# Kernel optimization log

Measured on AMD Instinct MI355X. Metric: run time of the kernel, lower is better.

Reference implementation:

```python
import jax, jax.numpy as jnp
import numpy as np

B, N, S, T_STEPS = 8, 150, 22, 1000
E = 2 * N - 1  # 299
M = 32


def quat_mul(a, b):
    # Hamilton product, quats as (w, x, y, z)
    aw, ax, ay, az = a[..., 0], a[..., 1], a[..., 2], a[..., 3]
    bw, bx, by, bz = b[..., 0], b[..., 1], b[..., 2], b[..., 3]
    return jnp.stack([
        aw * bw - ax * bx - ay * by - az * bz,
        aw * bx + ax * bw + ay * bz - az * by,
        aw * by - ax * bz + ay * bw + az * bx,
        aw * bz + ax * by - ay * bx + az * bw,
    ], axis=-1)


def quat_conj(q):
    return q * jnp.array([1.0, -1.0, -1.0, -1.0], q.dtype)


def quat_rotate(q, v):
    # rotate vector v by unit quaternion q
    w, qv = q[..., :1], q[..., 1:]
    t = 2.0 * jnp.cross(qv, v)
    return v + w * t + jnp.cross(qv, t)


def egnn_layer(q, x, h, e, mask_f, Wm, bm, Wf, bf, Wq, bq):
    Bb, Nn = h.shape[0], h.shape[-2]
    eye = jnp.eye(Nn, dtype=h.dtype)
    mm = mask_f[:, :, None] * mask_f[:, None, :] * (1.0 - eye)  # [B,N,N]
    n_nodes = mask_f.sum(-1)  # [B]
    q_i = q[:, :, None, :]
    q_j = q[:, None, :, :]
    x_i = x[:, :, None, :]
    x_j = x[:, None, :, :]
    qj_inv = quat_conj(q_j)
    diff = x_i - x_j                              # [B,N,N,3]
    local_x = quat_rotate(qj_inv, diff)           # R_j^T (x_i - x_j)
    local_q = quat_mul(quat_mul(qj_inv, q_i), q_j)  # q_j^-1 q_i q_j
    d2 = jnp.sum(diff * diff, -1)                 # [B,N,N]
    dot = jnp.abs(jnp.sum(q_i * q_j, -1))         # [B,N,N]
    hi = jnp.broadcast_to(h[:, :, None, :], (Bb, Nn, Nn, h.shape[-1]))
    hj = jnp.broadcast_to(h[:, None, :, :], (Bb, Nn, Nn, h.shape[-1]))
    feat = jnp.concatenate([hi, hj, e, local_x, local_q, d2[..., None], dot[..., None]], -1)
    m = (feat @ Wm + bm) * mm[..., None]          # [B,N,N,M]
    o = jnp.concatenate([h, m.sum(-2)], -1) @ Wf + bf
    delta = (m @ Wq + bq) * mm[..., None]         # [B,N,N,6]
    upd_x = (quat_rotate(q_j, local_x + delta[..., 3:]) + x_j).sum(-2) \
        / (n_nodes[:, None, None] - 1.0)
    vec_q = jnp.concatenate([jnp.zeros_like(delta[..., :1]), delta[..., :3]], -1)
    s = (local_q + quat_mul(local_q, vec_q)).sum(-2)  # [B,N,4]
    local_upd_q = s / jnp.maximum(jnp.linalg.norm(s, axis=-1, keepdims=True), 1e-12)
    upd_q = quat_mul(quat_mul(q, local_upd_q), quat_conj(q))
    return upd_q, upd_x, o


def relposenc():
    r = jnp.arange(N)
    rel = N - 1 + (r[:, None] - r[None, :])
    return jax.nn.one_hot(rel, E, dtype=jnp.float32)  # [N,N,E]


def setup_inputs() -> dict:
    key = jax.random.key(0)
    ks = jax.random.split(key, 32)
    quats = jax.random.normal(ks[0], (B, N, 4), dtype=jnp.float32)
    quats = quats / jnp.linalg.norm(quats, axis=-1, keepdims=True)
    trans = jax.random.normal(ks[1], (B, N, 3), dtype=jnp.float32) * 10.0
    features = jax.random.uniform(ks[2], (B, N, S), dtype=jnp.float32)
    mask = jnp.ones((B, N), dtype=bool)
    inp = {"quats": quats, "trans": trans, "features": features, "mask": mask, "t": 250}
    # (message_in, feature_in, feature_out) per layer; H1=30, I=64
    dims = [(2 * 30 + E + 9, 30 + M, 64), (2 * 64 + E + 9, 64 + M, 64),
            (2 * 64 + E + 9, 64 + M, 64), (2 * 64 + E + 9, 64 + M, 1)]
    k = 3
    for i, (mi, fi, fo) in enumerate(dims, 1):
        inp[f"wm{i}"] = jax.random.normal(ks[k], (mi, M), dtype=jnp.float32) / np.float32(np.sqrt(mi)); k += 1
        inp[f"bm{i}"] = jnp.zeros((M,), jnp.float32)
        inp[f"wf{i}"] = jax.random.normal(ks[k], (fi, fo), dtype=jnp.float32) / np.float32(np.sqrt(fi)); k += 1
        inp[f"bf{i}"] = jnp.zeros((fo,), jnp.float32)
        inp[f"wq{i}"] = jax.random.normal(ks[k], (M, 6), dtype=jnp.float32) / np.float32(np.sqrt(M)); k += 1
        inp[f"bq{i}"] = jnp.zeros((6,), jnp.float32)
    return inp


def reference(quats, trans, features,
              wm1, bm1, wf1, bf1, wq1, bq1,
              wm2, bm2, wf2, bf2, wq2, bq2,
              wm3, bm3, wf3, bf3, wq3, bq3,
              wm4, bm4, wf4, bf4, wq4, bq4,
              mask, t):
    mask_f = mask.astype(quats.dtype)
    ft = jnp.full((B, N, 1), t / T_STEPS, dtype=quats.dtype)
    h = jnp.concatenate([quats, trans, features, ft], -1)  # [B,N,30]
    e = jnp.broadcast_to(relposenc()[None], (B, N, N, E))
    q, x = quats, trans
    q, x, i1 = egnn_layer(q, x, h, e, mask_f, wm1, bm1, wf1, bf1, wq1, bq1)
    q, x, i2 = egnn_layer(q, x, jax.nn.relu(i1), e, mask_f, wm2, bm2, wf2, bf2, wq2, bq2)
    q, x, i3 = egnn_layer(q, x, jax.nn.relu(i2), e, mask_f, wm3, bm3, wf3, bf3, wq3, bq3)
    q, x, _ = egnn_layer(q, x, jax.nn.relu(i3), e, mask_f, wm4, bm4, wf4, bf4, wq4, bq4)
    return jnp.concatenate([q, x], -1)  # tensor_7 of final frames [B,N,7]
```

## Files before the change

kernel.cpp:

```cpp
#include <hip/hip_runtime.h>
#include <math.h>

#define NB 8
#define NN 150
#define NE 299
#define NNODE (NB*NN)

struct Quat { float w, x, y, z; };

__device__ inline Quat qmul(Quat a, Quat b) {
    Quat r;
    r.w = a.w*b.w - a.x*b.x - a.y*b.y - a.z*b.z;
    r.x = a.w*b.x + a.x*b.w + a.y*b.z - a.z*b.y;
    r.y = a.w*b.y - a.x*b.z + a.y*b.w + a.z*b.x;
    r.z = a.w*b.z + a.x*b.y - a.y*b.x + a.z*b.w;
    return r;
}
__device__ inline Quat qconj(Quat a) { return Quat{a.w, -a.x, -a.y, -a.z}; }

__device__ inline float3 qrot(Quat q, float3 v) {
    float tx = 2.f*(q.y*v.z - q.z*v.y);
    float ty = 2.f*(q.z*v.x - q.x*v.z);
    float tz = 2.f*(q.x*v.y - q.y*v.x);
    float cx = q.y*tz - q.z*ty;
    float cy = q.z*tx - q.x*tz;
    float cz = q.x*ty - q.y*tx;
    float3 r;
    r.x = v.x + q.w*tx + cx;
    r.y = v.y + q.w*ty + cy;
    r.z = v.z + q.w*tz + cz;
    return r;
}

struct InitArgs {
    const float* quats; const float* trans; const float* feats; const int* tptr;
    const float* wm[4]; const float* wq[4];
    const float* bm1; const float* bq1;
    float* h; float* A; float* C0; float* Ad; float* Cd0;
    float* P; float* Ed; float* Gq;
};

__global__ __launch_bounds__(256) void init_kernel(InitArgs a)
{
    __shared__ float sh[8][30];
    __shared__ float sA[8][32];
    __shared__ float sC[8][32];
    __shared__ float sPS[256];
    const int tid = threadIdx.x;
    const int blk = blockIdx.x;

    if (blk < 150) {
        const int nodeBase = blk*8;
        for (int idx = tid; idx < 8*30; idx += 256) {
            const int nl = idx / 30;
            const int d  = idx - nl*30;
            const int n  = nodeBase + nl;
            float v;
            if      (d < 4)  v = a.quats[n*4 + d];
            else if (d < 7)  v = a.trans[n*3 + (d-4)];
            else if (d < 29) v = a.feats[n*22 + (d-7)];
            else             v = (float)a.tptr[0] * (1.0f/1000.0f);
            sh[nl][d] = v;
            a.h[n*64 + d] = v;
        }
        __syncthreads();
        {
            const int nl = tid >> 5;
            const int k  = tid & 31;
            const int n  = nodeBase + nl;
            float av = a.bm1[k], cv = 0.f;
#pragma unroll
            for (int d = 0; d < 30; ++d) {
                const float hv = sh[nl][d];
                av = fmaf(hv, a.wm[0][d*32 + k], av);
                cv = fmaf(hv, a.wm[0][(30+d)*32 + k], cv);
            }
            a.A[n*32 + k]  = av;
            a.C0[n*32 + k] = cv;
            sA[nl][k] = av;
            sC[nl][k] = cv;
        }
        __syncthreads();
        if (tid < 96) {
            const int half = (tid >= 48) ? 1 : 0;
            const int idx  = tid - half*48;
            const int nl = idx / 6;
            const int d  = idx - nl*6;
            const float* src = half ? sC[nl] : sA[nl];
            float acc = half ? 0.f : a.bq1[d];
#pragma unroll
            for (int k = 0; k < 32; ++k) acc = fmaf(src[k], a.wq[0][k*6 + d], acc);
            (half ? a.Cd0 : a.Ad)[(nodeBase+nl)*8 + d] = acc;
        }
    } else if (blk < 154) {
        const int l = blk - 150;
        const int HDl = (l == 0) ? 30 : 64;
        const float* E = a.wm[l] + 2*HDl*32;
        float* Pl = a.P + l*9600;
        const int g = tid >> 5, k = tid & 31;
        const int r0 = g*38;
        float part = 0.f;
        for (int r = r0; r < r0+38 && r < NE; ++r) part += E[r*32 + k];
        sPS[g*32 + k] = part;
        __syncthreads();
        float run = 0.f;
        for (int gg = 0; gg < g; ++gg) run += sPS[gg*32 + k];
        const int rw = (r0+38 < 300) ? r0+38 : 300;
        for (int r = r0; r < rw; ++r) {
            Pl[r*32 + k] = run;
            if (r < NE) run += E[r*32 + k];
        }
    } else if (blk < 158) {
        const int l = blk - 154;
        const int HDl = (l == 0) ? 30 : 64;
        const float* E  = a.wm[l] + 2*HDl*32;
        const float* Wq = a.wq[l];
        if (tid < 54) {
            const int t = tid/6, d = tid - t*6;
            float acc = 0.f;
#pragma unroll
            for (int k = 0; k < 32; ++k) acc = fmaf(E[(NE+t)*32 + k], Wq[k*6 + d], acc);
            a.Gq[l*64 + t*6 + d] = acc;
        }
    } else {
        const int bb = blk - 158;
        const int l = bb / 25;
        const int rbase = (bb % 25) * 12;
        const int HDl = (l == 0) ? 30 : 64;
        const float* E  = a.wm[l] + 2*HDl*32;
        const float* Wq = a.wq[l];
        if (tid < 72) {
            const int rr = tid/6, d = tid - rr*6;
            const int r = rbase + rr;
            if (r < NE) {
                float acc = 0.f;
#pragma unroll
                for (int k = 0; k < 32; ++k) acc = fmaf(E[r*32 + k], Wq[k*6 + d], acc);
                a.Ed[l*2400 + r*8 + d] = acc;
            }
        }
    }
}

struct PairArgs {
    const float* qcur; const float* xcur;
    const float* hbuf; const float* Abuf;
    const float* Cin;  const float* Adin; const float* Cdin;
    const float* Ed;   const float* Gq;   const float* P;
    const float* wm;   const float* wf;   const float* bf;
    const float* wmN;  const float* bmN;
    const float* wqN;  const float* bqN;
    float* hout; float* Aout; float* Adout;
    float* Cout; float* Cdout;
    float* qout; float* xout; float* dout;
};

template<int HD, bool COMPUTE_O, bool WRITE_OUT>
__global__ __launch_bounds__(192, 4) void pair_kernel(PairArgs a)
{
    constexpr int STR  = 196;
    constexpr int NROW = COMPUTE_O ? 32 : 7;
    constexpr int NV   = COMPUTE_O ? 16 : 7;
    __shared__ __align__(16) float sMat[NROW*STR];
    __shared__ float sWmG[COMPUTE_O ? 288 : 4];
    __shared__ float sPr[192];
    __shared__ float sTot[16];
    __shared__ float sCs[32];
    __shared__ float sHi[64], sO[64], sMs[32];
    __shared__ float sGq[54], sAd[6];
    __shared__ float sA2[32], sC2[32];

    const int tid   = threadIdx.x;
    const int nodeI = blockIdx.x;
    const int b     = nodeI / NN;
    const int i     = nodeI - b*NN;

    if (COMPUTE_O) {
        for (int idx = tid; idx < 288; idx += 192) sWmG[idx] = a.wm[(2*HD+NE)*32 + idx];
        for (int idx = tid; idx < HD;  idx += 192) sHi[idx]  = a.hbuf[nodeI*64 + idx];
    }
    if (tid < 54) sGq[tid] = a.Gq[tid];
    if (tid >= 64 && tid < 70) sAd[tid-64] = a.Adin[nodeI*8 + (tid-64)];
    __syncthreads();

    const Quat  qi = {a.qcur[nodeI*4+0], a.qcur[nodeI*4+1],
                      a.qcur[nodeI*4+2], a.qcur[nodeI*4+3]};
    const float3 xi = {a.xcur[nodeI*3+0], a.xcur[nodeI*3+1], a.xcur[nodeI*3+2]};

    float vals[NV];
#pragma unroll
    for (int v = 0; v < NV; ++v) vals[v] = 0.f;

    const int j = tid;
    Quat qj = {1.f,0.f,0.f,0.f};
    const float mm = (j == i) ? 0.f : 1.f;
    if (j < NN) {
        const int nodeJ = b*NN + j;
        qj = Quat{a.qcur[nodeJ*4+0], a.qcur[nodeJ*4+1],
                  a.qcur[nodeJ*4+2], a.qcur[nodeJ*4+3]};
        float3 xj = {a.xcur[nodeJ*3+0], a.xcur[nodeJ*3+1], a.xcur[nodeJ*3+2]};
        float3 diff = {xi.x - xj.x, xi.y - xj.y, xi.z - xj.z};
        Quat qjc = qconj(qj);
        float3 lx = qrot(qjc, diff);
        Quat lq = qmul(qmul(qjc, qi), qj);
        const float d2 = diff.x*diff.x + diff.y*diff.y + diff.z*diff.z;
        const float dt = fabsf(qi.w*qj.w + qi.x*qj.x + qi.y*qj.y + qi.z*qj.z);
        const float g[9] = {lx.x, lx.y, lx.z, lq.w, lq.x, lq.y, lq.z, d2, dt};

        const float4* cd4 = (const float4*)(a.Cdin + nodeJ*8);
        const float4* ed4 = (const float4*)(a.Ed + (NN-1 + i - j)*8);
        const float4 c0 = cd4[0], c1 = cd4[1];
        const float4 e0 = ed4[0], e1 = ed4[1];
        float delta[6];
        delta[0] = sAd[0] + c0.x + e0.x;
        delta[1] = sAd[1] + c0.y + e0.y;
        delta[2] = sAd[2] + c0.z + e0.z;
        delta[3] = sAd[3] + c0.w + e0.w;
        delta[4] = sAd[4] + c1.x + e1.x;
        delta[5] = sAd[5] + c1.y + e1.y;
#pragma unroll
        for (int t = 0; t < 9; ++t) {
            const float gv = g[t];
#pragma unroll
            for (int d = 0; d < 6; ++d)
                delta[d] = fmaf(gv, sGq[t*6 + d], delta[d]);
        }
#pragma unroll
        for (int d = 0; d < 6; ++d) delta[d] *= mm;

        constexpr int vo = COMPUTE_O ? 9 : 0;
        if (COMPUTE_O) {
#pragma unroll
            for (int t = 0; t < 9; ++t) vals[t] = g[t]*mm;
        }
        float3 dv = {delta[3], delta[4], delta[5]};
        float3 rd = qrot(qj, dv);
        vals[vo+0] = rd.x; vals[vo+1] = rd.y; vals[vo+2] = rd.z;
        Quat vq = {0.f, delta[0], delta[1], delta[2]};
        Quat sp = qmul(lq, vq);
        vals[vo+3] = lq.w + sp.w;
        vals[vo+4] = lq.x + sp.x;
        vals[vo+5] = lq.y + sp.y;
        vals[vo+6] = lq.z + sp.z;
    }

#pragma unroll
    for (int v = 0; v < NV; ++v) sMat[v*STR + tid] = vals[v];
    if (COMPUTE_O) {
        if (j < NN) {
            const float4* c4p = (const float4*)(a.Cin + (b*NN+j)*32);
#pragma unroll
            for (int q = 0; q < 4; ++q) {
                const float4 c = c4p[q];
                sMat[(16+4*q+0)*STR + tid] = c.x*mm;
                sMat[(16+4*q+1)*STR + tid] = c.y*mm;
                sMat[(16+4*q+2)*STR + tid] = c.z*mm;
                sMat[(16+4*q+3)*STR + tid] = c.w*mm;
            }
        } else {
#pragma unroll
            for (int r = 16; r < 32; ++r) sMat[r*STR + tid] = 0.f;
        }
    }
    __syncthreads();
    if (tid < 4*NROW) {
        const int ch = tid >> 2, q4 = tid & 3;
        const float4* row = (const float4*)(sMat + ch*STR + q4*48);
        float s0 = 0.f, s1 = 0.f, s2 = 0.f, s3 = 0.f;
#pragma unroll
        for (int it = 0; it < 12; ++it) {
            const float4 r = row[it];
            s0 += r.x; s1 += r.y; s2 += r.z; s3 += r.w;
        }
        sPr[tid] = (s0+s1) + (s2+s3);
    }
    __syncthreads();

    if (COMPUTE_O) {
        if (j < NN) {
            const float4* c4p = (const float4*)(a.Cin + (b*NN+j)*32);
#pragma unroll
            for (int q = 0; q < 4; ++q) {
                const float4 c = c4p[4+q];
                sMat[(4*q+0)*STR + tid] = c.x*mm;
                sMat[(4*q+1)*STR + tid] = c.y*mm;
                sMat[(4*q+2)*STR + tid] = c.z*mm;
                sMat[(4*q+3)*STR + tid] = c.w*mm;
            }
        } else {
#pragma unroll
            for (int r = 0; r < 16; ++r) sMat[r*STR + tid] = 0.f;
        }
        __syncthreads();
        if (tid < 64) {
            const int ch = tid >> 2, q4 = tid & 3;
            const float4* row = (const float4*)(sMat + ch*STR + q4*48);
            float s0 = 0.f, s1 = 0.f, s2 = 0.f, s3 = 0.f;
#pragma unroll
            for (int it = 0; it < 12; ++it) {
                const float4 r = row[it];
                s0 += r.x; s1 += r.y; s2 += r.z; s3 += r.w;
            }
            sPr[128 + tid] = (s0+s1) + (s2+s3);
        }
        __syncthreads();
    }

    if (COMPUTE_O) {
        if (tid < 16)
            sTot[tid] = (sPr[4*tid] + sPr[4*tid+1]) + (sPr[4*tid+2] + sPr[4*tid+3]);
        else if (tid < 32) {
            const int c = tid - 16, o4 = 64 + 4*c;
            sCs[c] = (sPr[o4] + sPr[o4+1]) + (sPr[o4+2] + sPr[o4+3]);
        } else if (tid < 48) {
            const int c = tid - 16, o4 = 128 + 4*(tid-32);
            sCs[c] = (sPr[o4] + sPr[o4+1]) + (sPr[o4+2] + sPr[o4+3]);
        }
    } else {
        if (tid < 7)
            sTot[tid] = (sPr[4*tid] + sPr[4*tid+1]) + (sPr[4*tid+2] + sPr[4*tid+3]);
    }
    __syncthreads();

    if (COMPUTE_O) {
        if (tid < 32) {
            const int k = tid;
            float ms = 149.f*a.Abuf[nodeI*32 + k] + sCs[k]
                     + a.P[(i+NN)*32 + k] - a.P[i*32 + k]
                     - a.wm[(2*HD + (NN-1))*32 + k];
#pragma unroll
            for (int t = 0; t < 9; ++t) ms = fmaf(sTot[t], sWmG[t*32 + k], ms);
            sMs[k] = ms;
        }
        __syncthreads();
        if (tid < 64) {
            float acc0 = a.bf[tid], acc1 = 0.f;
#pragma unroll 8
            for (int d = 0; d < HD; d += 2) {
                acc0 = fmaf(sHi[d],   a.wf[d*64 + tid],     acc0);
                acc1 = fmaf(sHi[d+1], a.wf[(d+1)*64 + tid], acc1);
            }
#pragma unroll 8
            for (int k = 0; k < 32; k += 2) {
                acc0 = fmaf(sMs[k],   a.wf[(HD+k)*64 + tid],   acc0);
                acc1 = fmaf(sMs[k+1], a.wf[(HD+k+1)*64 + tid], acc1);
            }
            sO[tid] = acc0 + acc1;
        }
    }

    if (tid == 0) {
        constexpr int XO = COMPUTE_O ? 9 : 0;
        const float inv = 1.0f / (float)(NN - 1);
        const float ux0 = ((float)NN * xi.x + sTot[XO+0]) * inv;
        const float ux1 = ((float)NN * xi.y + sTot[XO+1]) * inv;
        const float ux2 = ((float)NN * xi.z + sTot[XO+2]) * inv;
        Quat s = {sTot[XO+3], sTot[XO+4], sTot[XO+5], sTot[XO+6]};
        const float nrm = sqrtf(s.w*s.w + s.x*s.x + s.y*s.y + s.z*s.z);
        const float invn = 1.0f / fmaxf(nrm, 1e-12f);
        Quat u = {s.w*invn, s.x*invn, s.y*invn, s.z*invn};
        Quat uq = qmul(qmul(qi, u), qconj(qi));
        if (WRITE_OUT) {
            float* op = a.dout + nodeI*7;
            op[0] = uq.w; op[1] = uq.x; op[2] = uq.y; op[3] = uq.z;
            op[4] = ux0;  op[5] = ux1;  op[6] = ux2;
        } else {
            a.qout[nodeI*4+0] = uq.w; a.qout[nodeI*4+1] = uq.x;
            a.qout[nodeI*4+2] = uq.y; a.qout[nodeI*4+3] = uq.z;
            a.xout[nodeI*3+0] = ux0;  a.xout[nodeI*3+1] = ux1;
            a.xout[nodeI*3+2] = ux2;
        }
    }

    if (COMPUTE_O) {
        __syncthreads();
        if (tid < 64) {
            const float hn = fmaxf(sO[tid], 0.f);
            sHi[tid] = hn;
            a.hout[nodeI*64 + tid] = hn;
        }
        __syncthreads();
        if (tid < 64) {
            const int k   = tid & 31;
            const int off = (tid >= 32) ? 64 : 0;
            float acc = (tid < 32) ? a.bmN[k] : 0.f;
#pragma unroll
            for (int d = 0; d < 64; ++d) acc = fmaf(sHi[d], a.wmN[(off+d)*32 + k], acc);
            if (tid < 32) { a.Aout[nodeI*32 + k] = acc; sA2[k] = acc; }
            else          { a.Cout[nodeI*32 + k] = acc; sC2[k] = acc; }
        }
        __syncthreads();
        if (tid < 12) {
            const int half = (tid >= 6) ? 1 : 0;
            const int d = tid - half*6;
            const float* src = half ? sC2 : sA2;
            float acc = half ? 0.f : a.bqN[d];
#pragma unroll
            for (int k = 0; k < 32; ++k) acc = fmaf(src[k], a.wqN[k*6 + d], acc);
            (half ? a.Cdout : a.Adout)[nodeI*8 + d] = acc;
        }
    }
}


extern "C" void kernel_launch(void* const* d_in, const int* in_sizes, int n_in,
                              void* d_out, int out_size, void* d_ws, size_t ws_size,
                              hipStream_t stream) {
    const float* wm[4] = {(const float*)d_in[5],  (const float*)d_in[11],
                          (const float*)d_in[17], (const float*)d_in[23]};
    const float* bm[4] = {(const float*)d_in[6],  (const float*)d_in[12],
                          (const float*)d_in[18], (const float*)d_in[24]};
    const float* wf[4] = {(const float*)d_in[7],  (const float*)d_in[13],
                          (const float*)d_in[19], (const float*)d_in[25]};
    const float* bf[4] = {(const float*)d_in[8],  (const float*)d_in[14],
                          (const float*)d_in[20], (const float*)d_in[26]};
    const float* wq[4] = {(const float*)d_in[9],  (const float*)d_in[15],
                          (const float*)d_in[21], (const float*)d_in[27]};
    const float* bq[4] = {(const float*)d_in[10], (const float*)d_in[16],
                          (const float*)d_in[22], (const float*)d_in[28]};

    float* ws = (float*)d_ws;
    float* h   = ws;
    float* A   = h   + NNODE*64;
    float* C0  = A   + NNODE*32;
    float* C1  = C0  + NNODE*32;
    float* Ad  = C1  + NNODE*32;
    float* Cd0 = Ad  + NNODE*8;
    float* Cd1 = Cd0 + NNODE*8;
    float* qA  = Cd1 + NNODE*8;
    float* xA  = qA  + NNODE*4;
    float* qB  = xA  + NNODE*3;
    float* xB  = qB  + NNODE*4;
    float* Pp  = xB  + NNODE*3;
    float* Edp = Pp  + 4*9600;
    float* Gqp = Edp + 4*2400;

    InitArgs ia;
    ia.quats = (const float*)d_in[0];
    ia.trans = (const float*)d_in[1];
    ia.feats = (const float*)d_in[2];
    ia.tptr  = (const int*)d_in[4];
    for (int l = 0; l < 4; ++l) { ia.wm[l] = wm[l]; ia.wq[l] = wq[l]; }
    ia.bm1 = bm[0]; ia.bq1 = bq[0];
    ia.h = h; ia.A = A; ia.C0 = C0; ia.Ad = Ad; ia.Cd0 = Cd0;
    ia.P = Pp; ia.Ed = Edp; ia.Gq = Gqp;
    init_kernel<<<dim3(258), dim3(256), 0, stream>>>(ia);

    PairArgs p;
    p.hout = h; p.Aout = A; p.Adout = Ad;
    p.dout = (float*)d_out;

    p.qcur = (const float*)d_in[0]; p.xcur = (const float*)d_in[1];
    p.hbuf = h; p.Abuf = A; p.Cin = C0; p.Adin = Ad; p.Cdin = Cd0;
    p.Ed = Edp + 0*2400; p.Gq = Gqp + 0*64; p.P = Pp + 0*9600;
    p.wm = wm[0]; p.wf = wf[0]; p.bf = bf[0];
    p.wmN = wm[1]; p.bmN = bm[1]; p.wqN = wq[1]; p.bqN = bq[1];
    p.Cout = C1; p.Cdout = Cd1;
    p.qout = qA; p.xout = xA;
    pair_kernel<30, true, false><<<dim3(NNODE), dim3(192), 0, stream>>>(p);

    p.qcur = qA; p.xcur = xA;
    p.Cin = C1; p.Cdin = Cd1;
    p.Ed = Edp + 1*2400; p.Gq = Gqp + 1*64; p.P = Pp + 1*9600;
    p.wm = wm[1]; p.wf = wf[1]; p.bf = bf[1];
    p.wmN = wm[2]; p.bmN = bm[2]; p.wqN = wq[2]; p.bqN = bq[2];
    p.Cout = C0; p.Cdout = Cd0;
    p.qout = qB; p.xout = xB;
    pair_kernel<64, true, false><<<dim3(NNODE), dim3(192), 0, stream>>>(p);

    p.qcur = qB; p.xcur = xB;
    p.Cin = C0; p.Cdin = Cd0;
    p.Ed = Edp + 2*2400; p.Gq = Gqp + 2*64; p.P = Pp + 2*9600;
    p.wm = wm[2]; p.wf = wf[2]; p.bf = bf[2];
    p.wmN = wm[3]; p.bmN = bm[3]; p.wqN = wq[3]; p.bqN = bq[3];
    p.Cout = C1; p.Cdout = Cd1;
    p.qout = qA; p.xout = xA;
    pair_kernel<64, true, false><<<dim3(NNODE), dim3(192), 0, stream>>>(p);

    p.qcur = qA; p.xcur = xA;
    p.Cin = C1; p.Cdin = Cd1;
    p.Ed = Edp + 3*2400; p.Gq = Gqp + 3*64; p.P = Pp + 3*9600;
    p.wm = wm[3]; p.wf = wf[3]; p.bf = bf[3];
    p.wmN = wm[3]; p.bmN = bm[3]; p.wqN = wq[3]; p.bqN = bq[3];
    p.Cout = C0; p.Cdout = Cd0;
    p.qout = nullptr; p.xout = nullptr;
    pair_kernel<64, false, true><<<dim3(NNODE), dim3(192), 0, stream>>>(p);
}
```

Before: 167.5 us.

## Fold init kernel into first pair kernel and precompute next-layer tables in-line

```diff
diff --git a/kernel.cpp b/kernel.cpp
--- a/kernel.cpp
+++ b/kernel.cpp
@@ -32,130 +32,22 @@
     return r;
 }
 
-struct InitArgs {
-    const float* quats; const float* trans; const float* feats; const int* tptr;
-    const float* wm[4]; const float* wq[4];
-    const float* bm1; const float* bq1;
-    float* h; float* A; float* C0; float* Ad; float* Cd0;
-    float* P; float* Ed; float* Gq;
-};
-
-__global__ __launch_bounds__(256) void init_kernel(InitArgs a)
-{
-    __shared__ float sh[8][30];
-    __shared__ float sA[8][32];
-    __shared__ float sC[8][32];
-    __shared__ float sPS[256];
-    const int tid = threadIdx.x;
-    const int blk = blockIdx.x;
-
-    if (blk < 150) {
-        const int nodeBase = blk*8;
-        for (int idx = tid; idx < 8*30; idx += 256) {
-            const int nl = idx / 30;
-            const int d  = idx - nl*30;
-            const int n  = nodeBase + nl;
-            float v;
-            if      (d < 4)  v = a.quats[n*4 + d];
-            else if (d < 7)  v = a.trans[n*3 + (d-4)];
-            else if (d < 29) v = a.feats[n*22 + (d-7)];
-            else             v = (float)a.tptr[0] * (1.0f/1000.0f);
-            sh[nl][d] = v;
-            a.h[n*64 + d] = v;
-        }
-        __syncthreads();
-        {
-            const int nl = tid >> 5;
-            const int k  = tid & 31;
-            const int n  = nodeBase + nl;
-            float av = a.bm1[k], cv = 0.f;
-#pragma unroll
-            for (int d = 0; d < 30; ++d) {
-                const float hv = sh[nl][d];
-                av = fmaf(hv, a.wm[0][d*32 + k], av);
-                cv = fmaf(hv, a.wm[0][(30+d)*32 + k], cv);
-            }
-            a.A[n*32 + k]  = av;
-            a.C0[n*32 + k] = cv;
-            sA[nl][k] = av;
-            sC[nl][k] = cv;
-        }
-        __syncthreads();
-        if (tid < 96) {
-            const int half = (tid >= 48) ? 1 : 0;
-            const int idx  = tid - half*48;
-            const int nl = idx / 6;
-            const int d  = idx - nl*6;
-            const float* src = half ? sC[nl] : sA[nl];
-            float acc = half ? 0.f : a.bq1[d];
-#pragma unroll
-            for (int k = 0; k < 32; ++k) acc = fmaf(src[k], a.wq[0][k*6 + d], acc);
-            (half ? a.Cd0 : a.Ad)[(nodeBase+nl)*8 + d] = acc;
-        }
-    } else if (blk < 154) {
-        const int l = blk - 150;
-        const int HDl = (l == 0) ? 30 : 64;
-        const float* E = a.wm[l] + 2*HDl*32;
-        float* Pl = a.P + l*9600;
-        const int g = tid >> 5, k = tid & 31;
-        const int r0 = g*38;
-        float part = 0.f;
-        for (int r = r0; r < r0+38 && r < NE; ++r) part += E[r*32 + k];
-        sPS[g*32 + k] = part;
-        __syncthreads();
-        float run = 0.f;
-        for (int gg = 0; gg < g; ++gg) run += sPS[gg*32 + k];
-        const int rw = (r0+38 < 300) ? r0+38 : 300;
-        for (int r = r0; r < rw; ++r) {
-            Pl[r*32 + k] = run;
-            if (r < NE) run += E[r*32 + k];
-        }
-    } else if (blk < 158) {
-        const int l = blk - 154;
-        const int HDl = (l == 0) ? 30 : 64;
-        const float* E  = a.wm[l] + 2*HDl*32;
-        const float* Wq = a.wq[l];
-        if (tid < 54) {
-            const int t = tid/6, d = tid - t*6;
-            float acc = 0.f;
-#pragma unroll
-            for (int k = 0; k < 32; ++k) acc = fmaf(E[(NE+t)*32 + k], Wq[k*6 + d], acc);
-            a.Gq[l*64 + t*6 + d] = acc;
-        }
-    } else {
-        const int bb = blk - 158;
-        const int l = bb / 25;
-        const int rbase = (bb % 25) * 12;
-        const int HDl = (l == 0) ? 30 : 64;
-        const float* E  = a.wm[l] + 2*HDl*32;
-        const float* Wq = a.wq[l];
-        if (tid < 72) {
-            const int rr = tid/6, d = tid - rr*6;
-            const int r = rbase + rr;
-            if (r < NE) {
-                float acc = 0.f;
-#pragma unroll
-                for (int k = 0; k < 32; ++k) acc = fmaf(E[r*32 + k], Wq[k*6 + d], acc);
-                a.Ed[l*2400 + r*8 + d] = acc;
-            }
-        }
-    }
-}
-
 struct PairArgs {
     const float* qcur; const float* xcur;
+    const float* feats; const int* tptr;
     const float* hbuf; const float* Abuf;
     const float* Cin;  const float* Adin; const float* Cdin;
     const float* Ed;   const float* Gq;   const float* P;
-    const float* wm;   const float* wf;   const float* bf;
-    const float* wmN;  const float* bmN;
-    const float* wqN;  const float* bqN;
+    const float* wm;   const float* bmT;  const float* wqT; const float* bqT;
+    const float* wf;   const float* bf;
+    const float* wmN;  const float* bmN;  const float* wqN; const float* bqN;
     float* hout; float* Aout; float* Adout;
     float* Cout; float* Cdout;
+    float* PN; float* EdN; float* GqN;
     float* qout; float* xout; float* dout;
 };
 
-template<int HD, bool COMPUTE_O, bool WRITE_OUT>
+template<int HD, bool COMPUTE_O, bool WRITE_OUT, bool FIRST>
 __global__ __launch_bounds__(192, 4) void pair_kernel(PairArgs a)
 {
     constexpr int STR  = 196;
@@ -169,64 +61,162 @@
     __shared__ float sHi[64], sO[64], sMs[32];
     __shared__ float sGq[54], sAd[6];
     __shared__ float sA2[32], sC2[32];
+    __shared__ float sWq[FIRST ? 192 : 1];
+    __shared__ float sWmC[FIRST ? 960 : 1];
+    __shared__ float sEtot[FIRST ? 32 : 1];
 
     const int tid   = threadIdx.x;
     const int nodeI = blockIdx.x;
     const int b     = nodeI / NN;
     const int i     = nodeI - b*NN;
+    const int j     = tid;
+    const float* Etab = a.wm + 2*HD*32;
 
     if (COMPUTE_O) {
         for (int idx = tid; idx < 288; idx += 192) sWmG[idx] = a.wm[(2*HD+NE)*32 + idx];
-        for (int idx = tid; idx < HD;  idx += 192) sHi[idx]  = a.hbuf[nodeI*64 + idx];
-    }
-    if (tid < 54) sGq[tid] = a.Gq[tid];
-    if (tid >= 64 && tid < 70) sAd[tid-64] = a.Adin[nodeI*8 + (tid-64)];
+        if (!FIRST)
+            for (int idx = tid; idx < HD; idx += 192) sHi[idx] = a.hbuf[nodeI*64 + idx];
+    }
+    if (FIRST) {
+        sWq[tid] = a.wqT[tid];
+        for (int idx = tid; idx < 960; idx += 192) sWmC[idx] = a.wm[HD*32 + idx];
+        if (tid < 30) {
+            float v;
+            if      (tid < 4)  v = a.qcur[nodeI*4 + tid];
+            else if (tid < 7)  v = a.xcur[nodeI*3 + (tid-4)];
+            else if (tid < 29) v = a.feats[nodeI*22 + (tid-7)];
+            else               v = (float)a.tptr[0] * (1.0f/1000.0f);
+            sHi[tid] = v;
+        }
+    } else {
+        if (tid < 54) sGq[tid] = a.Gq[tid];
+        if (tid < 6)  sAd[tid] = a.Adin[nodeI*8 + tid];
+    }
     __syncthreads();
 
-    const Quat  qi = {a.qcur[nodeI*4+0], a.qcur[nodeI*4+1],
-                      a.qcur[nodeI*4+2], a.qcur[nodeI*4+3]};
+    const float4 qi4 = ((const float4*)a.qcur)[nodeI];
+    const Quat  qi = {qi4.x, qi4.y, qi4.z, qi4.w};
     const float3 xi = {a.xcur[nodeI*3+0], a.xcur[nodeI*3+1], a.xcur[nodeI*3+2]};
 
+    const bool act = (j < NN);
+    const int nodeJ = b*NN + j;
+    const float mm = (j == i) ? 0.f : 1.f;
+
+    Quat qj = {1.f,0.f,0.f,0.f};
+    float3 xj = {0.f,0.f,0.f};
+    float cj[FIRST ? 32 : 1];
+    float cdj6[FIRST ? 6 : 1];
+
+    if (FIRST) {
+        if (act) {
+            float hj[30];
+            const float4 q4 = ((const float4*)a.qcur)[nodeJ];
+            hj[0]=q4.x; hj[1]=q4.y; hj[2]=q4.z; hj[3]=q4.w;
+            hj[4]=a.xcur[nodeJ*3+0]; hj[5]=a.xcur[nodeJ*3+1]; hj[6]=a.xcur[nodeJ*3+2];
+#pragma unroll
+            for (int d2 = 0; d2 < 22; ++d2) hj[7+d2] = a.feats[nodeJ*22 + d2];
+            hj[29] = (float)a.tptr[0] * (1.0f/1000.0f);
+            qj = Quat{hj[0],hj[1],hj[2],hj[3]};
+            xj = float3{hj[4],hj[5],hj[6]};
+#pragma unroll
+            for (int k = 0; k < 32; ++k) cj[k] = 0.f;
+#pragma unroll
+            for (int d2 = 0; d2 < 30; ++d2) {
+                const float hv = hj[d2];
+#pragma unroll
+                for (int k = 0; k < 32; ++k) cj[k] = fmaf(hv, sWmC[d2*32+k], cj[k]);
+            }
+#pragma unroll
+            for (int d2 = 0; d2 < 6; ++d2) {
+                float acc = 0.f;
+#pragma unroll
+                for (int k = 0; k < 32; ++k) acc = fmaf(cj[k], sWq[k*6+d2], acc);
+                cdj6[d2] = acc;
+            }
+        }
+        if (tid < 32) {
+            float acc = a.bmT[tid];
+#pragma unroll
+            for (int d2 = 0; d2 < 30; ++d2) acc = fmaf(sHi[d2], a.wm[d2*32+tid], acc);
+            sA2[tid] = acc;
+        }
+        if (tid >= 150) {
+            for (int tt = tid-150; tt < 54; tt += 42) {
+                const int tr = tt/6, dd = tt - tr*6;
+                float acc = 0.f;
+#pragma unroll
+                for (int k = 0; k < 32; ++k) acc = fmaf(Etab[(NE+tr)*32+k], sWq[k*6+dd], acc);
+                sGq[tt] = acc;
+            }
+        }
+        if (tid >= 160) {
+            const int k = tid-160;
+            float acc = -Etab[(NN-1)*32 + k];
+            for (int r = i; r < i+NN; ++r) acc += Etab[r*32 + k];
+            sEtot[k] = acc;
+        }
+        __syncthreads();
+        if (tid < 6) {
+            float acc = a.bqT[tid];
+#pragma unroll
+            for (int k = 0; k < 32; ++k) acc = fmaf(sA2[k], sWq[k*6+tid], acc);
+            sAd[tid] = acc;
+        }
+        __syncthreads();
+    } else {
+        if (act) {
+            const float4 q4 = ((const float4*)a.qcur)[nodeJ];
+            qj = Quat{q4.x, q4.y, q4.z, q4.w};
+            xj = float3{a.xcur[nodeJ*3+0], a.xcur[nodeJ*3+1], a.xcur[nodeJ*3+2]};
+        }
+    }
+
     float vals[NV];
 #pragma unroll
     for (int v = 0; v < NV; ++v) vals[v] = 0.f;
 
-    const int j = tid;
-    Quat qj = {1.f,0.f,0.f,0.f};
-    const float mm = (j == i) ? 0.f : 1.f;
-    if (j < NN) {
-        const int nodeJ = b*NN + j;
-        qj = Quat{a.qcur[nodeJ*4+0], a.qcur[nodeJ*4+1],
-                  a.qcur[nodeJ*4+2], a.qcur[nodeJ*4+3]};
-        float3 xj = {a.xcur[nodeJ*3+0], a.xcur[nodeJ*3+1], a.xcur[nodeJ*3+2]};
+    if (act) {
         float3 diff = {xi.x - xj.x, xi.y - xj.y, xi.z - xj.z};
         Quat qjc = qconj(qj);
         float3 lx = qrot(qjc, diff);
         Quat lq = qmul(qmul(qjc, qi), qj);
-        const float d2 = diff.x*diff.x + diff.y*diff.y + diff.z*diff.z;
+        const float d2v = diff.x*diff.x + diff.y*diff.y + diff.z*diff.z;
         const float dt = fabsf(qi.w*qj.w + qi.x*qj.x + qi.y*qj.y + qi.z*qj.z);
-        const float g[9] = {lx.x, lx.y, lx.z, lq.w, lq.x, lq.y, lq.z, d2, dt};
-
-        const float4* cd4 = (const float4*)(a.Cdin + nodeJ*8);
-        const float4* ed4 = (const float4*)(a.Ed + (NN-1 + i - j)*8);
-        const float4 c0 = cd4[0], c1 = cd4[1];
-        const float4 e0 = ed4[0], e1 = ed4[1];
+        const float g[9] = {lx.x, lx.y, lx.z, lq.w, lq.x, lq.y, lq.z, d2v, dt};
+
         float delta[6];
-        delta[0] = sAd[0] + c0.x + e0.x;
-        delta[1] = sAd[1] + c0.y + e0.y;
-        delta[2] = sAd[2] + c0.z + e0.z;
-        delta[3] = sAd[3] + c0.w + e0.w;
-        delta[4] = sAd[4] + c1.x + e1.x;
-        delta[5] = sAd[5] + c1.y + e1.y;
+        if (FIRST) {
+#pragma unroll
+            for (int d2 = 0; d2 < 6; ++d2) delta[d2] = sAd[d2] + cdj6[d2];
+            const float* Er = Etab + (NN-1 + i - j)*32;
+#pragma unroll
+            for (int k = 0; k < 32; ++k) {
+                const float ev = Er[k];
+#pragma unroll
+                for (int d2 = 0; d2 < 6; ++d2)
+                    delta[d2] = fmaf(ev, sWq[k*6+d2], delta[d2]);
+            }
+        } else {
+            const float4* cd4 = (const float4*)(a.Cdin + nodeJ*8);
+            const float4* ed4 = (const float4*)(a.Ed + (NN-1 + i - j)*8);
+            const float4 c0 = cd4[0], c1 = cd4[1];
+            const float4 e0 = ed4[0], e1 = ed4[1];
+            delta[0] = sAd[0] + c0.x + e0.x;
+            delta[1] = sAd[1] + c0.y + e0.y;
+            delta[2] = sAd[2] + c0.z + e0.z;
+            delta[3] = sAd[3] + c0.w + e0.w;
+            delta[4] = sAd[4] + c1.x + e1.x;
+            delta[5] = sAd[5] + c1.y + e1.y;
+        }
 #pragma unroll
         for (int t = 0; t < 9; ++t) {
             const float gv = g[t];
 #pragma unroll
-            for (int d = 0; d < 6; ++d)
-                delta[d] = fmaf(gv, sGq[t*6 + d], delta[d]);
-        }
-#pragma unroll
-        for (int d = 0; d < 6; ++d) delta[d] *= mm;
+            for (int d2 = 0; d2 < 6; ++d2)
+                delta[d2] = fmaf(gv, sGq[t*6 + d2], delta[d2]);
+        }
+#pragma unroll
+        for (int d2 = 0; d2 < 6; ++d2) delta[d2] *= mm;
 
         constexpr int vo = COMPUTE_O ? 9 : 0;
         if (COMPUTE_O) {
@@ -247,19 +237,29 @@
 #pragma unroll
     for (int v = 0; v < NV; ++v) sMat[v*STR + tid] = vals[v];
     if (COMPUTE_O) {
-        if (j < NN) {
-            const float4* c4p = (const float4*)(a.Cin + (b*NN+j)*32);
-#pragma unroll
-            for (int q = 0; q < 4; ++q) {
-                const float4 c = c4p[q];
-                sMat[(16+4*q+0)*STR + tid] = c.x*mm;
-                sMat[(16+4*q+1)*STR + tid] = c.y*mm;
-                sMat[(16+4*q+2)*STR + tid] = c.z*mm;
-                sMat[(16+4*q+3)*STR + tid] = c.w*mm;
+        if (FIRST) {
+            if (act) {
+#pragma unroll
+                for (int r = 0; r < 16; ++r) sMat[(16+r)*STR + tid] = cj[r]*mm;
+            } else {
+#pragma unroll
+                for (int r = 16; r < 32; ++r) sMat[r*STR + tid] = 0.f;
             }
         } else {
-#pragma unroll
-            for (int r = 16; r < 32; ++r) sMat[r*STR + tid] = 0.f;
+            if (act) {
+                const float4* c4p = (const float4*)(a.Cin + nodeJ*32);
+#pragma unroll
+                for (int q = 0; q < 4; ++q) {
+                    const float4 c = c4p[q];
+                    sMat[(16+4*q+0)*STR + tid] = c.x*mm;
+                    sMat[(16+4*q+1)*STR + tid] = c.y*mm;
+                    sMat[(16+4*q+2)*STR + tid] = c.z*mm;
+                    sMat[(16+4*q+3)*STR + tid] = c.w*mm;
+                }
+            } else {
+#pragma unroll
+                for (int r = 16; r < 32; ++r) sMat[r*STR + tid] = 0.f;
+            }
         }
     }
     __syncthreads();
@@ -277,19 +277,29 @@
     __syncthreads();
 
     if (COMPUTE_O) {
-        if (j < NN) {
-            const float4* c4p = (const float4*)(a.Cin + (b*NN+j)*32);
-#pragma unroll
-            for (int q = 0; q < 4; ++q) {
-                const float4 c = c4p[4+q];
-                sMat[(4*q+0)*STR + tid] = c.x*mm;
-                sMat[(4*q+1)*STR + tid] = c.y*mm;
-                sMat[(4*q+2)*STR + tid] = c.z*mm;
-                sMat[(4*q+3)*STR + tid] = c.w*mm;
+        if (FIRST) {
+            if (act) {
+#pragma unroll
+                for (int r = 0; r < 16; ++r) sMat[r*STR + tid] = cj[16+r]*mm;
+            } else {
+#pragma unroll
+                for (int r = 0; r < 16; ++r) sMat[r*STR + tid] = 0.f;
             }
         } else {
-#pragma unroll
-            for (int r = 0; r < 16; ++r) sMat[r*STR + tid] = 0.f;
+            if (act) {
+                const float4* c4p = (const float4*)(a.Cin + nodeJ*32);
+#pragma unroll
+                for (int q = 0; q < 4; ++q) {
+                    const float4 c = c4p[4+q];
+                    sMat[(4*q+0)*STR + tid] = c.x*mm;
+                    sMat[(4*q+1)*STR + tid] = c.y*mm;
+                    sMat[(4*q+2)*STR + tid] = c.z*mm;
+                    sMat[(4*q+3)*STR + tid] = c.w*mm;
+                }
+            } else {
+#pragma unroll
+                for (int r = 0; r < 16; ++r) sMat[r*STR + tid] = 0.f;
+            }
         }
         __syncthreads();
         if (tid < 64) {
@@ -325,9 +335,13 @@
     if (COMPUTE_O) {
         if (tid < 32) {
             const int k = tid;
-            float ms = 149.f*a.Abuf[nodeI*32 + k] + sCs[k]
-                     + a.P[(i+NN)*32 + k] - a.P[i*32 + k]
-                     - a.wm[(2*HD + (NN-1))*32 + k];
+            float ms;
+            if (FIRST)
+                ms = 149.f*sA2[k] + sCs[k] + sEtot[k];
+            else
+                ms = 149.f*a.Abuf[nodeI*32 + k] + sCs[k]
+                   + a.P[(i+NN)*32 + k] - a.P[i*32 + k]
+                   - a.wm[(2*HD + (NN-1))*32 + k];
 #pragma unroll
             for (int t = 0; t < 9; ++t) ms = fmaf(sTot[t], sWmG[t*32 + k], ms);
             sMs[k] = ms;
@@ -336,9 +350,9 @@
         if (tid < 64) {
             float acc0 = a.bf[tid], acc1 = 0.f;
 #pragma unroll 8
-            for (int d = 0; d < HD; d += 2) {
-                acc0 = fmaf(sHi[d],   a.wf[d*64 + tid],     acc0);
-                acc1 = fmaf(sHi[d+1], a.wf[(d+1)*64 + tid], acc1);
+            for (int d2 = 0; d2 < HD; d2 += 2) {
+                acc0 = fmaf(sHi[d2],   a.wf[d2*64 + tid],     acc0);
+                acc1 = fmaf(sHi[d2+1], a.wf[(d2+1)*64 + tid], acc1);
             }
 #pragma unroll 8
             for (int k = 0; k < 32; k += 2) {
@@ -385,19 +399,50 @@
             const int off = (tid >= 32) ? 64 : 0;
             float acc = (tid < 32) ? a.bmN[k] : 0.f;
 #pragma unroll
-            for (int d = 0; d < 64; ++d) acc = fmaf(sHi[d], a.wmN[(off+d)*32 + k], acc);
+            for (int d2 = 0; d2 < 64; ++d2) acc = fmaf(sHi[d2], a.wmN[(off+d2)*32 + k], acc);
             if (tid < 32) { a.Aout[nodeI*32 + k] = acc; sA2[k] = acc; }
             else          { a.Cout[nodeI*32 + k] = acc; sC2[k] = acc; }
         }
         __syncthreads();
         if (tid < 12) {
             const int half = (tid >= 6) ? 1 : 0;
-            const int d = tid - half*6;
+            const int d2 = tid - half*6;
             const float* src = half ? sC2 : sA2;
-            float acc = half ? 0.f : a.bqN[d];
-#pragma unroll
-            for (int k = 0; k < 32; ++k) acc = fmaf(src[k], a.wqN[k*6 + d], acc);
-            (half ? a.Cdout : a.Adout)[nodeI*8 + d] = acc;
+            float acc = half ? 0.f : a.bqN[d2];
+#pragma unroll
+            for (int k = 0; k < 32; ++k) acc = fmaf(src[k], a.wqN[k*6 + d2], acc);
+            (half ? a.Cdout : a.Adout)[nodeI*8 + d2] = acc;
+        }
+
+        const float* EN = a.wmN + 2*64*32;
+        if (nodeI < NE && tid >= 64 && tid < 70) {
+            const int dd = tid - 64;
+            float acc = 0.f;
+#pragma unroll
+            for (int k = 0; k < 32; ++k) acc = fmaf(EN[nodeI*32+k], a.wqN[k*6+dd], acc);
+            a.EdN[nodeI*8+dd] = acc;
+        }
+        if (nodeI == 1100 && tid >= 64 && tid < 118) {
+            const int tt = tid-64; const int tr = tt/6, dd = tt - tr*6;
+            float acc = 0.f;
+#pragma unroll
+            for (int k = 0; k < 32; ++k) acc = fmaf(EN[(NE+tr)*32+k], a.wqN[k*6+dd], acc);
+            a.GqN[tr*6+dd] = acc;
+        }
+        if (nodeI == 1101) {
+            __syncthreads();
+            const int gp = tid >> 5, k = tid & 31;
+            const int r0 = gp*50;
+            float part = 0.f;
+            for (int r = r0; r < r0+50 && r < NE; ++r) part += EN[r*32 + k];
+            sPr[gp*32 + k] = part;
+            __syncthreads();
+            float run = 0.f;
+            for (int gg = 0; gg < gp; ++gg) run += sPr[gg*32 + k];
+            for (int r = r0; r < r0+50; ++r) {
+                a.PN[r*32 + k] = run;
+                if (r < NE) run += EN[r*32 + k];
+            }
         }
     }
 }
@@ -406,6 +451,8 @@
 extern "C" void kernel_launch(void* const* d_in, const int* in_sizes, int n_in,
                               void* d_out, int out_size, void* d_ws, size_t ws_size,
                               hipStream_t stream) {
+    const float* quats = (const float*)d_in[0];
+    const float* trans = (const float*)d_in[1];
     const float* wm[4] = {(const float*)d_in[5],  (const float*)d_in[11],
                           (const float*)d_in[17], (const float*)d_in[23]};
     const float* bm[4] = {(const float*)d_in[6],  (const float*)d_in[12],
@@ -422,12 +469,12 @@
     float* ws = (float*)d_ws;
     float* h   = ws;
     float* A   = h   + NNODE*64;
-    float* C0  = A   + NNODE*32;
-    float* C1  = C0  + NNODE*32;
-    float* Ad  = C1  + NNODE*32;
-    float* Cd0 = Ad  + NNODE*8;
-    float* Cd1 = Cd0 + NNODE*8;
-    float* qA  = Cd1 + NNODE*8;
+    float* CA  = A   + NNODE*32;
+    float* CB  = CA  + NNODE*32;
+    float* Ad  = CB  + NNODE*32;
+    float* CdA = Ad  + NNODE*8;
+    float* CdB = CdA + NNODE*8;
+    float* qA  = CdB + NNODE*8;
     float* xA  = qA  + NNODE*4;
     float* qB  = xA  + NNODE*3;
     float* xB  = qB  + NNODE*4;
@@ -435,54 +482,51 @@
     float* Edp = Pp  + 4*9600;
     float* Gqp = Edp + 4*2400;
 
-    InitArgs ia;
-    ia.quats = (const float*)d_in[0];
-    ia.trans = (const float*)d_in[1];
-    ia.feats = (const float*)d_in[2];
-    ia.tptr  = (const int*)d_in[4];
-    for (int l = 0; l < 4; ++l) { ia.wm[l] = wm[l]; ia.wq[l] = wq[l]; }
-    ia.bm1 = bm[0]; ia.bq1 = bq[0];
-    ia.h = h; ia.A = A; ia.C0 = C0; ia.Ad = Ad; ia.Cd0 = Cd0;
-    ia.P = Pp; ia.Ed = Edp; ia.Gq = Gqp;
-    init_kernel<<<dim3(258), dim3(256), 0, stream>>>(ia);
-
     PairArgs p;
-    p.hout = h; p.Aout = A; p.Adout = Ad;
-    p.dout = (float*)d_out;
-
-    p.qcur = (const float*)d_in[0]; p.xcur = (const float*)d_in[1];
-    p.hbuf = h; p.Abuf = A; p.Cin = C0; p.Adin = Ad; p.Cdin = Cd0;
-    p.Ed = Edp + 0*2400; p.Gq = Gqp + 0*64; p.P = Pp + 0*9600;
-    p.wm = wm[0]; p.wf = wf[0]; p.bf = bf[0];
+    p.feats = (const float*)d_in[2];
+    p.tptr  = (const int*)d_in[4];
+    p.dout  = (float*)d_out;
+
+    p.qcur = quats; p.xcur = trans;
+    p.hbuf = nullptr; p.Abuf = nullptr; p.Cin = nullptr;
+    p.Adin = nullptr; p.Cdin = nullptr;
+    p.Ed = nullptr; p.Gq = nullptr; p.P = nullptr;
+    p.wm = wm[0]; p.bmT = bm[0]; p.wqT = wq[0]; p.bqT = bq[0];
+    p.wf = wf[0]; p.bf = bf[0];
     p.wmN = wm[1]; p.bmN = bm[1]; p.wqN = wq[1]; p.bqN = bq[1];
-    p.Cout = C1; p.Cdout = Cd1;
+    p.hout = h; p.Aout = A; p.Adout = Ad; p.Cout = CA; p.Cdout = CdA;
+    p.PN = Pp + 1*9600; p.EdN = Edp + 1*2400; p.GqN = Gqp + 1*64;
     p.qout = qA; p.xout = xA;
-    pair_kernel<30, true, false><<<dim3(NNODE), dim3(192), 0, stream>>>(p);
+    pair_kernel<30, true, false, true><<<dim3(NNODE), dim3(192), 0, stream>>>(p);
 
     p.qcur = qA; p.xcur = xA;
-    p.Cin = C1; p.Cdin = Cd1;
+    p.hbuf = h; p.Abuf = A; p.Cin = CA; p.Adin = Ad; p.Cdin = CdA;
     p.Ed = Edp + 1*2400; p.Gq = Gqp + 1*64; p.P = Pp + 1*9600;
-    p.wm = wm[1]; p.wf = wf[1]; p.bf = bf[1];
+    p.wm = wm[1]; p.bmT = bm[1]; p.wqT = wq[1]; p.bqT = bq[1];
+    p.wf = wf[1]; p.bf = bf[1];
     p.wmN = wm[2]; p.bmN = bm[2]; p.wqN = wq[2]; p.bqN = bq[2];
-    p.Cout = C0; p.Cdout = Cd0;
+    p.Cout = CB; p.Cdout = CdB;
+    p.PN = Pp + 2*9600; p.EdN = Edp + 2*2400; p.GqN = Gqp + 2*64;
     p.qout = qB; p.xout = xB;
-    pair_kernel<64, true, false><<<dim3(NNODE), dim3(192), 0, stream>>>(p);
+    pair_kernel<64, true, false, false><<<dim3(NNODE), dim3(192), 0, stream>>>(p);
 
     p.qcur = qB; p.xcur = xB;
-    p.Cin = C0; p.Cdin = Cd0;
+    p.Cin = CB; p.Cdin = CdB;
     p.Ed = Edp + 2*2400; p.Gq = Gqp + 2*64; p.P = Pp + 2*9600;
-    p.wm = wm[2]; p.wf = wf[2]; p.bf = bf[2];
+    p.wm = wm[2]; p.bmT = bm[2]; p.wqT = wq[2]; p.bqT = bq[2];
+    p.wf = wf[2]; p.bf = bf[2];
     p.wmN = wm[3]; p.bmN = bm[3]; p.wqN = wq[3]; p.bqN = bq[3];
-    p.Cout = C1; p.Cdout = Cd1;
+    p.Cout = CA; p.Cdout = CdA;
+    p.PN = Pp + 3*9600; p.EdN = Edp + 3*2400; p.GqN = Gqp + 3*64;
     p.qout = qA; p.xout = xA;
-    pair_kernel<64, true, false><<<dim3(NNODE), dim3(192), 0, stream>>>(p);
+    pair_kernel<64, true, false, false><<<dim3(NNODE), dim3(192), 0, stream>>>(p);
 
     p.qcur = qA; p.xcur = xA;
-    p.Cin = C1; p.Cdin = Cd1;
+    p.Cin = CA; p.Cdin = CdA; p.Adin = Ad;
     p.Ed = Edp + 3*2400; p.Gq = Gqp + 3*64; p.P = Pp + 3*9600;
-    p.wm = wm[3]; p.wf = wf[3]; p.bf = bf[3];
+    p.wm = wm[3]; p.bmT = bm[3]; p.wqT = wq[3]; p.bqT = bq[3];
+    p.wf = wf[3]; p.bf = bf[3];
     p.wmN = wm[3]; p.bmN = bm[3]; p.wqN = wq[3]; p.bqN = bq[3];
-    p.Cout = C0; p.Cdout = Cd0;
     p.qout = nullptr; p.xout = nullptr;
-    pair_kernel<64, false, true><<<dim3(NNODE), dim3(192), 0, stream>>>(p);
+    pair_kernel<64, false, true, false><<<dim3(NNODE), dim3(192), 0, stream>>>(p);
 }
```

After: 242.6 us. +44.8%, slower.
